# Performance work log

Measured on AMD Instinct MI355X. Metric: run time of the kernel, lower is better.

## Reference

```python
import jax, jax.numpy as jnp
import numpy as np

N = 500000          # number of nodes/points
Q = 64              # Q_mesoscale quadrature points
XI_MIN, XI_MAX = 0.0, 70.0
MLP_DIMS = [3, 64, 64, 64, 64, 1]  # num_layers=5, hidden_dim=64
STOP = 1e-3
MAX_ITER = 100


def setup_inputs() -> dict:
    key = jax.random.key(0)
    ks = jax.random.split(key, 3 + 2 * (len(MLP_DIMS) - 1))
    inp = {
        "f_distribution": jax.random.uniform(ks[0], (N, Q), jnp.float32),
        "macro_features": jax.random.uniform(ks[1], (N, 2), jnp.float32),
        "position_embedding": jax.random.normal(ks[2], (N, 1), jnp.float32),
    }
    for i in range(len(MLP_DIMS) - 1):
        din, dout = MLP_DIMS[i], MLP_DIMS[i + 1]
        scale = 1.0 / np.sqrt(din)
        inp[f"W{i}"] = jax.random.uniform(ks[3 + 2 * i], (dout, din), jnp.float32, -scale, scale)
        inp[f"b{i}"] = jax.random.uniform(ks[4 + 2 * i], (dout,), jnp.float32, -scale, scale)
    return inp


def _solve_lambda_mu(v, xi, xi2, stop=STOP, max_iter=MAX_ITER):
    # Newton-Raphson for exponential-family equilibrium: find lambda s.t. S1/S0 == v.
    # v: [N,1], xi/xi2: [Q]. Runs entirely on-device via lax.while_loop.
    def moments(lam):
        w = jnp.exp(lam * xi)                 # [N,Q]
        S0 = w.sum(axis=1, keepdims=True)     # [N,1]
        S1 = (w * xi).sum(axis=1, keepdims=True)
        S2 = (w * xi2).sum(axis=1, keepdims=True)
        return S0, S1, S2

    lam0 = jnp.zeros_like(v)
    S0, S1, S2 = moments(lam0)
    gp = (S0 * S2 - S1 ** 2) / S0 ** 2        # variance (Newton denominator)

    def cond(state):
        i, lam, S0, S1, gp = state
        return (i < max_iter) & (jnp.max(jnp.abs(gp)) > stop)

    def body(state):
        i, lam, S0, S1, gp = state
        lam1 = lam - (S1 / S0 - v) / gp
        S0, S1, S2 = moments(lam1)
        gp = (S0 * S2 - S1 ** 2) / S0 ** 2
        return (i + 1, lam1, S0, S1, gp)

    _, lam, S0, _, _ = jax.lax.while_loop(cond, body, (0, lam0, S0, S1, gp))
    mu0 = -jnp.log(S0)
    return lam, mu0


def _tau_mlp(x, Ws, bs):
    for i, (W, b) in enumerate(zip(Ws, bs)):
        x = x @ W.T + b
        if i < len(Ws) - 1:
            x = jnp.tanh(x)
    return jnp.exp(x)  # tau [N,1]


def reference(f_distribution, macro_features, position_embedding,
              W0, b0, W1, b1, W2, b2, W3, b3, W4, b4):
    xi = jnp.linspace(XI_MIN, XI_MAX, f_distribution.shape[1]).astype(f_distribution.dtype)
    rho = f_distribution.mean(axis=1, keepdims=True)                 # [N,1]
    lam, mu0 = _solve_lambda_mu(macro_features[:, :1], xi, xi * xi)  # [N,1] each
    f_eq = rho * jnp.exp(mu0) * jnp.exp(lam * xi)                    # [N,Q]
    x = jnp.concatenate([macro_features, position_embedding], axis=-1)  # [N,3]
    tau = _tau_mlp(x, [W0, W1, W2, W3, W4], [b0, b1, b2, b3, b4])    # [N,1]
    omega = -(f_distribution - f_eq) / tau                           # [N,Q]
    return omega
```

## Files before the change

### kernel.cpp

```cpp
#include <hip/hip_runtime.h>
#include <math.h>

#define Q 64
#define NPB 256

typedef __attribute__((ext_vector_type(8))) short bf16x8;
typedef __attribute__((ext_vector_type(16))) float f32x16;
typedef __attribute__((ext_vector_type(4))) unsigned int u32x4;

union BFr { u32x4 u; bf16x8 v; };

#define MFMA32(a, b, cc) __builtin_amdgcn_mfma_f32_32x32x16_bf16(a, b, cc, 0, 0, 0)

__device__ __forceinline__ float pade_tanh(float x) {
    float xc = fminf(fmaxf(x, -4.4f), 4.4f);
    float t  = xc * xc;
    float p  = fmaf(t, fmaf(t, 21.0f, 1260.0f), 10395.0f);
    float q  = fmaf(t, fmaf(t, t + 210.0f, 4725.0f), 10395.0f);
    return (xc * p) * __builtin_amdgcn_rcpf(q);
}

__device__ __forceinline__ unsigned short bf16rne(float x) {
    unsigned u = __float_as_uint(x);
    return (unsigned short)((u + 0x7fffu + ((u >> 16) & 1u)) >> 16);
}

__device__ __forceinline__ void bf16split(float x, unsigned short& h, unsigned short& l) {
    h = bf16rne(x);
    float rest = x - __uint_as_float(((unsigned)h) << 16);
    l = bf16rne(rest);
}

__device__ __forceinline__ unsigned cvt_pk_bf16(float lo, float hi) {
    unsigned r;
    asm("v_cvt_pk_bf16_f32 %0, %1, %2" : "=v"(r) : "v"(lo), "v"(hi));
    return r;
}

__device__ __forceinline__ float sum16_dpp(float x) {
    x += __int_as_float(__builtin_amdgcn_update_dpp(0, __float_as_int(x), 0xB1,  0xF, 0xF, true));
    x += __int_as_float(__builtin_amdgcn_update_dpp(0, __float_as_int(x), 0x4E,  0xF, 0xF, true));
    x += __int_as_float(__builtin_amdgcn_update_dpp(0, __float_as_int(x), 0x124, 0xF, 0xF, true));
    x += __int_as_float(__builtin_amdgcn_update_dpp(0, __float_as_int(x), 0x128, 0xF, 0xF, true));
    return x;
}

__global__ __launch_bounds__(256)
void build_wfrag(const float* __restrict__ W0, const float* __restrict__ b0,
                 const float* __restrict__ W1, const float* __restrict__ W2,
                 const float* __restrict__ W3, unsigned short* __restrict__ ws)
{
    int idx = blockIdx.x * 256 + threadIdx.x;
    if (idx < 1536) {
        int L = idx >> 9, rem = idx & 511;
        int mtp = rem >> 8, s = (rem >> 6) & 3, lane = rem & 63;
        const float* W = (L == 0) ? W1 : (L == 1) ? W2 : W3;
        int n = 32 * mtp + (lane & 31);
        int hh2 = lane >> 5;
        #pragma unroll
        for (int i = 0; i < 8; ++i) {
            int k = 16 * s + 8 * hh2 + i;
            unsigned short hh, ll;
            bf16split(W[n * 64 + k], hh, ll);
            ws[idx * 8 + i] = hh;
            ws[12288 + idx * 8 + i] = ll;
        }
    } else if (idx < 1664) {
        int j = idx - 1536;
        int mtp = j >> 6, lane = j & 63;
        int n = 32 * mtp + (lane & 31);
        int hh2 = lane >> 5;
        #pragma unroll
        for (int i = 0; i < 8; ++i) {
            int k = 8 * hh2 + i;
            float v = (k < 3) ? W0[n * 3 + k] : ((k == 3) ? b0[n] : 0.0f);
            unsigned short hh, ll;
            bf16split(v, hh, ll);
            ws[24576 + j * 8 + i] = hh;
            ws[25600 + j * 8 + i] = ll;
        }
    }
}

#define BUILD_FRAGS(fr)                                               \
    BFr fr[4][2];                                                     \
    _Pragma("unroll")                                                 \
    for (int nt = 0; nt < 2; ++nt) {                                  \
        _Pragma("unroll")                                             \
        for (int s = 0; s < 4; ++s) {                                 \
            const int mt = s >> 1, e = 4 * (s & 1);                   \
            unsigned x1 = pk[mt][nt][e + 0], y1 = pk[mt][nt][e + 2];  \
            unsigned x2 = pk[mt][nt][e + 1], y2 = pk[mt][nt][e + 3];  \
            asm("v_permlane32_swap_b32 %0, %1" : "+v"(x1), "+v"(y1)); \
            asm("v_permlane32_swap_b32 %0, %1" : "+v"(x2), "+v"(y2)); \
            fr[s][nt].u = (u32x4){x1, x2, y1, y2};                    \
        }                                                             \
    }

__global__ __launch_bounds__(NPB, 4)
void bgk_mfma(const float* __restrict__ f,
              const float* __restrict__ macro,
              const float* __restrict__ pos,
              const float* __restrict__ b1,
              const float* __restrict__ b2,
              const float* __restrict__ b3,
              const float* __restrict__ W4,
              const float* __restrict__ b4,
              const unsigned short* __restrict__ ws,
              float* __restrict__ out, int n_nodes)
{
    __shared__ float4 s_prm[NPB];

    const int tid = threadIdx.x;
    const int wv = tid >> 6, lane = tid & 63;
    const int c5 = lane & 31, h = lane >> 5;
    const int nbase = blockIdx.x * NPB;
    const float XI_H = 70.0f / 63.0f;

    const int sub = lane >> 4;
    const int qi = (lane & 15) * 4;
    const int wbase = nbase + (wv << 6);
    float4 pre[8];
    #pragma unroll
    for (int k = 0; k < 8; ++k) {
        int n = wbase + k * 4 + sub;
        int ncl = (n < n_nodes) ? n : (n_nodes - 1);
        pre[k] = *(const float4*)(f + (size_t)ncl * Q + qi);
    }

    float lam, mu0, rgeo;
    {
        int n1 = nbase + tid;
        int nc2 = (n1 < n_nodes) ? n1 : (n_nodes - 1);
        float m0 = macro[nc2 * 2];
        rgeo = fmaxf(m0 / (m0 + XI_H), 1e-30f);
        float lr = logf(rgeo);
        lam = lr / XI_H;
        float r64 = __expf(64.0f * lr);
        mu0 = -logf((1.0f - r64) / (1.0f - rgeo));
    }

    const bf16x8* wAh = (const bf16x8*)(ws);
    const bf16x8* wAl = (const bf16x8*)(ws + 12288);
    const bf16x8* l0h = (const bf16x8*)(ws + 24576);
    const bf16x8* l0l = (const bf16x8*)(ws + 25600);
    const f32x16 zero16 = {0,0,0,0,0,0,0,0,0,0,0,0,0,0,0,0};

    unsigned pk[2][2][8];

    {
        BFr bh[2], bl[2];
        #pragma unroll
        for (int nt = 0; nt < 2; ++nt) {
            int node = nbase + (wv << 6) + 32 * nt + c5;
            if (node >= n_nodes) node = n_nodes - 1;
            float m0 = macro[node * 2], m1 = macro[node * 2 + 1], pp = pos[node];
            unsigned short h0, l0_, h1, l1_, h2, l2_;
            bf16split(m0, h0, l0_); bf16split(m1, h1, l1_); bf16split(pp, h2, l2_);
            unsigned w0h = (unsigned)h0 | ((unsigned)h1 << 16);
            unsigned w1h = (unsigned)h2 | (0x3F80u << 16);
            unsigned w0l = (unsigned)l0_ | ((unsigned)l1_ << 16);
            unsigned w1l = (unsigned)l2_;
            bh[nt].u = (u32x4){ h ? 0u : w0h, h ? 0u : w1h, 0u, 0u };
            bl[nt].u = (u32x4){ h ? 0u : w0l, h ? 0u : w1l, 0u, 0u };
        }
        #pragma unroll
        for (int mtp = 0; mtp < 2; ++mtp) {
            bf16x8 Ah = l0h[mtp * 64 + lane];
            bf16x8 Al = l0l[mtp * 64 + lane];
            #pragma unroll
            for (int nt = 0; nt < 2; ++nt) {
                f32x16 t = zero16;
                t = MFMA32(Ah, bh[nt].v, t);
                t = MFMA32(Al, bh[nt].v, t);
                t = MFMA32(Ah, bl[nt].v, t);
                #pragma unroll
                for (int p = 0; p < 8; ++p)
                    pk[mtp][nt][p] = cvt_pk_bf16(pade_tanh(t[2 * p]), pade_tanh(t[2 * p + 1]));
            }
        }
    }

#define HIDDEN(Lc, BIAS)                                                       \
    {                                                                          \
        BUILD_FRAGS(fr)                                                        \
        _Pragma("unroll")                                                      \
        for (int mtp = 0; mtp < 2; ++mtp) {                                    \
            f32x16 a0;                                                         \
            _Pragma("unroll")                                                  \
            for (int j = 0; j < 4; ++j) {                                      \
                float4 bv = *(const float4*)&(BIAS)[32 * mtp + 8 * j + 4 * h]; \
                a0[4 * j + 0] = bv.x; a0[4 * j + 1] = bv.y;                    \
                a0[4 * j + 2] = bv.z; a0[4 * j + 3] = bv.w;                    \
            }                                                                  \
            f32x16 a1 = a0;                                                    \
            _Pragma("unroll")                                                  \
            for (int s = 0; s < 4; ++s) {                                      \
                const int fo = (((Lc) * 2 + mtp) * 4 + s) * 64 + lane;         \
                bf16x8 Ah = wAh[fo], Al = wAl[fo];                             \
                a0 = MFMA32(Ah, fr[s][0].v, a0);                               \
                a0 = MFMA32(Al, fr[s][0].v, a0);                               \
                a1 = MFMA32(Ah, fr[s][1].v, a1);                               \
                a1 = MFMA32(Al, fr[s][1].v, a1);                               \
            }                                                                  \
            _Pragma("unroll")                                                  \
            for (int j = 0; j < 4; ++j) {                                      \
                float v0 = pade_tanh(a0[4 * j + 0]);                           \
                float v1 = pade_tanh(a0[4 * j + 1]);                           \
                float v2 = pade_tanh(a0[4 * j + 2]);                           \
                float v3 = pade_tanh(a0[4 * j + 3]);                           \
                pk[mtp][0][2 * j + 0] = cvt_pk_bf16(v0, v1);                   \
                pk[mtp][0][2 * j + 1] = cvt_pk_bf16(v2, v3);                   \
                float u0 = pade_tanh(a1[4 * j + 0]);                           \
                float u1 = pade_tanh(a1[4 * j + 1]);                           \
                float u2 = pade_tanh(a1[4 * j + 2]);                           \
                float u3 = pade_tanh(a1[4 * j + 3]);                           \
                pk[mtp][1][2 * j + 0] = cvt_pk_bf16(u0, u1);                   \
                pk[mtp][1][2 * j + 1] = cvt_pk_bf16(u2, u3);                   \
            }                                                                  \
        }                                                                      \
    }

    HIDDEN(0, b1)
    HIDDEN(1, b2)

    {
        BUILD_FRAGS(fr)
        float zp0 = 0.f, zp1 = 0.f;
        #pragma unroll
        for (int mtp = 0; mtp < 2; ++mtp) {
            f32x16 a0;
            #pragma unroll
            for (int j = 0; j < 4; ++j) {
                float4 bv = *(const float4*)&b3[32 * mtp + 8 * j + 4 * h];
                a0[4 * j + 0] = bv.x; a0[4 * j + 1] = bv.y;
                a0[4 * j + 2] = bv.z; a0[4 * j + 3] = bv.w;
            }
            f32x16 a1 = a0;
            #pragma unroll
            for (int s = 0; s < 4; ++s) {
                const int fo = ((2 * 2 + mtp) * 4 + s) * 64 + lane;
                bf16x8 Ah = wAh[fo], Al = wAl[fo];
                a0 = MFMA32(Ah, fr[s][0].v, a0);
                a0 = MFMA32(Al, fr[s][0].v, a0);
                a1 = MFMA32(Ah, fr[s][1].v, a1);
                a1 = MFMA32(Al, fr[s][1].v, a1);
            }
            #pragma unroll
            for (int j = 0; j < 4; ++j) {
                float4 w4v = *(const float4*)&W4[32 * mtp + 8 * j + 4 * h];
                zp0 = fmaf(w4v.x, pade_tanh(a0[4 * j + 0]), zp0);
                zp0 = fmaf(w4v.y, pade_tanh(a0[4 * j + 1]), zp0);
                zp0 = fmaf(w4v.z, pade_tanh(a0[4 * j + 2]), zp0);
                zp0 = fmaf(w4v.w, pade_tanh(a0[4 * j + 3]), zp0);
                zp1 = fmaf(w4v.x, pade_tanh(a1[4 * j + 0]), zp1);
                zp1 = fmaf(w4v.y, pade_tanh(a1[4 * j + 1]), zp1);
                zp1 = fmaf(w4v.z, pade_tanh(a1[4 * j + 2]), zp1);
                zp1 = fmaf(w4v.w, pade_tanh(a1[4 * j + 3]), zp1);
            }
        }
        const float b4s = b4[0];
        zp0 += __shfl_xor(zp0, 32, 64);
        zp1 += __shfl_xor(zp1, 32, 64);
        float it0 = __expf(-(zp0 + b4s));
        float it1 = __expf(-(zp1 + b4s));
        float it  = h ? it1 : it0;
        s_prm[tid] = (float4){ it, lam, mu0, rgeo };
    }

    const float x0 = (float)qi * XI_H;
    {
        float4 fr2[8];
        #pragma unroll
        for (int k = 0; k < 8; ++k) {
            int n = wbase + (8 + k) * 4 + sub;
            int ncl = (n < n_nodes) ? n : (n_nodes - 1);
            fr2[k] = *(const float4*)(f + (size_t)ncl * Q + qi);
        }
        #pragma unroll
        for (int kb = 0; kb < 2; ++kb) {
            #pragma unroll
            for (int k = 0; k < 8; ++k) {
                const int local = (kb * 8 + k) * 4 + sub;
                const int n = wbase + local;
                const float4 fv = kb ? fr2[k] : pre[k];

                const float s = sum16_dpp(fv.x + fv.y + fv.z + fv.w);
                const float rho = s * (1.0f / 64.0f);

                const float4 prm = s_prm[(wv << 6) + local];

                const float e0 = rho * __expf(fmaf(prm.y, x0, prm.z));
                const float e1 = e0 * prm.w;
                const float e2 = e1 * prm.w;
                const float e3 = e2 * prm.w;

                float4 o;
                o.x = (e0 - fv.x) * prm.x;
                o.y = (e1 - fv.y) * prm.x;
                o.z = (e2 - fv.z) * prm.x;
                o.w = (e3 - fv.w) * prm.x;

                if (n < n_nodes) *(float4*)(out + (size_t)n * Q + qi) = o;
            }
        }
    }
}

extern "C" void kernel_launch(void* const* d_in, const int* in_sizes, int n_in,
                              void* d_out, int out_size, void* d_ws, size_t ws_size,
                              hipStream_t stream) {
    const float* f     = (const float*)d_in[0];
    const float* macro = (const float*)d_in[1];
    const float* pos   = (const float*)d_in[2];
    const float* W0 = (const float*)d_in[3];  const float* b0 = (const float*)d_in[4];
    const float* W1 = (const float*)d_in[5];  const float* b1 = (const float*)d_in[6];
    const float* W2 = (const float*)d_in[7];  const float* b2 = (const float*)d_in[8];
    const float* W3 = (const float*)d_in[9];  const float* b3 = (const float*)d_in[10];
    const float* W4 = (const float*)d_in[11]; const float* b4 = (const float*)d_in[12];
    float* out = (float*)d_out;
    unsigned short* ws = (unsigned short*)d_ws;

    const int n_nodes = in_sizes[0] / Q;
    build_wfrag<<<7, 256, 0, stream>>>(W0, b0, W1, W2, W3, ws);

    const int blocks = (n_nodes + NPB - 1) / NPB;
    bgk_mfma<<<blocks, NPB, 0, stream>>>(f, macro, pos,
                                         b1, b2, b3, W4, b4, ws,
                                         out, n_nodes);
}
```

Before: 84.06 us.

## Use single-wave blocks and pair tanh reciprocals to share one rcp

Shrinks each block from four waves to one wave of 64 nodes and drops the per-wave indexing, so blocks are smaller and can be scheduled more finely. The Pade tanh is evaluated two values at a time, with one reciprocal of the product of the denominators shared between them, which cuts the number of rcp instructions in the MLP epilogues. Combining the denominators can slightly change rounding or overflow behaviour for large inputs, although the inputs are clamped. Smaller blocks also mean four times as many blocks to launch, and the launch-bounds occupancy hint now covers far fewer threads per CU.

```diff
diff --git a/kernel.cpp b/kernel.cpp
--- a/kernel.cpp
+++ b/kernel.cpp
@@ -2,7 +2,7 @@
 #include <math.h>
 
 #define Q 64
-#define NPB 256
+#define NPB 64
 
 typedef __attribute__((ext_vector_type(8))) short bf16x8;
 typedef __attribute__((ext_vector_type(16))) float f32x16;
@@ -12,12 +12,17 @@
 
 #define MFMA32(a, b, cc) __builtin_amdgcn_mfma_f32_32x32x16_bf16(a, b, cc, 0, 0, 0)
 
-__device__ __forceinline__ float pade_tanh(float x) {
-    float xc = fminf(fmaxf(x, -4.4f), 4.4f);
-    float t  = xc * xc;
-    float p  = fmaf(t, fmaf(t, 21.0f, 1260.0f), 10395.0f);
-    float q  = fmaf(t, fmaf(t, t + 210.0f, 4725.0f), 10395.0f);
-    return (xc * p) * __builtin_amdgcn_rcpf(q);
+__device__ __forceinline__ void pade_tanh2(float x0, float x1, float& y0, float& y1) {
+    float c0 = fminf(fmaxf(x0, -4.4f), 4.4f);
+    float c1 = fminf(fmaxf(x1, -4.4f), 4.4f);
+    float t0 = c0 * c0, t1 = c1 * c1;
+    float p0 = fmaf(t0, fmaf(t0, 21.0f, 1260.0f), 10395.0f);
+    float p1 = fmaf(t1, fmaf(t1, 21.0f, 1260.0f), 10395.0f);
+    float q0 = fmaf(t0, fmaf(t0, t0 + 210.0f, 4725.0f), 10395.0f);
+    float q1 = fmaf(t1, fmaf(t1, t1 + 210.0f, 4725.0f), 10395.0f);
+    float rq = __builtin_amdgcn_rcpf(q0 * q1);
+    y0 = (c0 * p0) * (rq * q1);
+    y1 = (c1 * p1) * (rq * q0);
 }
 
 __device__ __forceinline__ unsigned short bf16rne(float x) {
@@ -111,26 +116,24 @@
 {
     __shared__ float4 s_prm[NPB];
 
-    const int tid = threadIdx.x;
-    const int wv = tid >> 6, lane = tid & 63;
+    const int lane = threadIdx.x & 63;
     const int c5 = lane & 31, h = lane >> 5;
     const int nbase = blockIdx.x * NPB;
     const float XI_H = 70.0f / 63.0f;
 
     const int sub = lane >> 4;
     const int qi = (lane & 15) * 4;
-    const int wbase = nbase + (wv << 6);
     float4 pre[8];
     #pragma unroll
     for (int k = 0; k < 8; ++k) {
-        int n = wbase + k * 4 + sub;
+        int n = nbase + k * 4 + sub;
         int ncl = (n < n_nodes) ? n : (n_nodes - 1);
         pre[k] = *(const float4*)(f + (size_t)ncl * Q + qi);
     }
 
     float lam, mu0, rgeo;
     {
-        int n1 = nbase + tid;
+        int n1 = nbase + lane;
         int nc2 = (n1 < n_nodes) ? n1 : (n_nodes - 1);
         float m0 = macro[nc2 * 2];
         rgeo = fmaxf(m0 / (m0 + XI_H), 1e-30f);
@@ -152,7 +155,7 @@
         BFr bh[2], bl[2];
         #pragma unroll
         for (int nt = 0; nt < 2; ++nt) {
-            int node = nbase + (wv << 6) + 32 * nt + c5;
+            int node = nbase + 32 * nt + c5;
             if (node >= n_nodes) node = n_nodes - 1;
             float m0 = macro[node * 2], m1 = macro[node * 2 + 1], pp = pos[node];
             unsigned short h0, l0_, h1, l1_, h2, l2_;
@@ -175,8 +178,11 @@
                 t = MFMA32(Al, bh[nt].v, t);
                 t = MFMA32(Ah, bl[nt].v, t);
                 #pragma unroll
-                for (int p = 0; p < 8; ++p)
-                    pk[mtp][nt][p] = cvt_pk_bf16(pade_tanh(t[2 * p]), pade_tanh(t[2 * p + 1]));
+                for (int p = 0; p < 8; ++p) {
+                    float y0, y1;
+                    pade_tanh2(t[2 * p], t[2 * p + 1], y0, y1);
+                    pk[mtp][nt][p] = cvt_pk_bf16(y0, y1);
+                }
             }
         }
     }
@@ -205,16 +211,14 @@
             }                                                                  \
             _Pragma("unroll")                                                  \
             for (int j = 0; j < 4; ++j) {                                      \
-                float v0 = pade_tanh(a0[4 * j + 0]);                           \
-                float v1 = pade_tanh(a0[4 * j + 1]);                           \
-                float v2 = pade_tanh(a0[4 * j + 2]);                           \
-                float v3 = pade_tanh(a0[4 * j + 3]);                           \
+                float v0, v1, v2, v3;                                          \
+                pade_tanh2(a0[4 * j + 0], a0[4 * j + 1], v0, v1);              \
+                pade_tanh2(a0[4 * j + 2], a0[4 * j + 3], v2, v3);              \
                 pk[mtp][0][2 * j + 0] = cvt_pk_bf16(v0, v1);                   \
                 pk[mtp][0][2 * j + 1] = cvt_pk_bf16(v2, v3);                   \
-                float u0 = pade_tanh(a1[4 * j + 0]);                           \
-                float u1 = pade_tanh(a1[4 * j + 1]);                           \
-                float u2 = pade_tanh(a1[4 * j + 2]);                           \
-                float u3 = pade_tanh(a1[4 * j + 3]);                           \
+                float u0, u1, u2, u3;                                          \
+                pade_tanh2(a1[4 * j + 0], a1[4 * j + 1], u0, u1);              \
+                pade_tanh2(a1[4 * j + 2], a1[4 * j + 3], u2, u3);              \
                 pk[mtp][1][2 * j + 0] = cvt_pk_bf16(u0, u1);                   \
                 pk[mtp][1][2 * j + 1] = cvt_pk_bf16(u2, u3);                   \
             }                                                                  \
@@ -249,14 +253,20 @@
             #pragma unroll
             for (int j = 0; j < 4; ++j) {
                 float4 w4v = *(const float4*)&W4[32 * mtp + 8 * j + 4 * h];
-                zp0 = fmaf(w4v.x, pade_tanh(a0[4 * j + 0]), zp0);
-                zp0 = fmaf(w4v.y, pade_tanh(a0[4 * j + 1]), zp0);
-                zp0 = fmaf(w4v.z, pade_tanh(a0[4 * j + 2]), zp0);
-                zp0 = fmaf(w4v.w, pade_tanh(a0[4 * j + 3]), zp0);
-                zp1 = fmaf(w4v.x, pade_tanh(a1[4 * j + 0]), zp1);
-                zp1 = fmaf(w4v.y, pade_tanh(a1[4 * j + 1]), zp1);
-                zp1 = fmaf(w4v.z, pade_tanh(a1[4 * j + 2]), zp1);
-                zp1 = fmaf(w4v.w, pade_tanh(a1[4 * j + 3]), zp1);
+                float s0, s1, s2, s3;
+                pade_tanh2(a0[4 * j + 0], a0[4 * j + 1], s0, s1);
+                pade_tanh2(a0[4 * j + 2], a0[4 * j + 3], s2, s3);
+                zp0 = fmaf(w4v.x, s0, zp0);
+                zp0 = fmaf(w4v.y, s1, zp0);
+                zp0 = fmaf(w4v.z, s2, zp0);
+                zp0 = fmaf(w4v.w, s3, zp0);
+                float r0, r1, r2, r3;
+                pade_tanh2(a1[4 * j + 0], a1[4 * j + 1], r0, r1);
+                pade_tanh2(a1[4 * j + 2], a1[4 * j + 3], r2, r3);
+                zp1 = fmaf(w4v.x, r0, zp1);
+                zp1 = fmaf(w4v.y, r1, zp1);
+                zp1 = fmaf(w4v.z, r2, zp1);
+                zp1 = fmaf(w4v.w, r3, zp1);
             }
         }
         const float b4s = b4[0];
@@ -265,7 +275,7 @@
         float it0 = __expf(-(zp0 + b4s));
         float it1 = __expf(-(zp1 + b4s));
         float it  = h ? it1 : it0;
-        s_prm[tid] = (float4){ it, lam, mu0, rgeo };
+        s_prm[lane] = (float4){ it, lam, mu0, rgeo };
     }
 
     const float x0 = (float)qi * XI_H;
@@ -273,7 +283,7 @@
         float4 fr2[8];
         #pragma unroll
         for (int k = 0; k < 8; ++k) {
-            int n = wbase + (8 + k) * 4 + sub;
+            int n = nbase + (8 + k) * 4 + sub;
             int ncl = (n < n_nodes) ? n : (n_nodes - 1);
             fr2[k] = *(const float4*)(f + (size_t)ncl * Q + qi);
         }
@@ -282,13 +292,13 @@
             #pragma unroll
             for (int k = 0; k < 8; ++k) {
                 const int local = (kb * 8 + k) * 4 + sub;
-                const int n = wbase + local;
+                const int n = nbase + local;
                 const float4 fv = kb ? fr2[k] : pre[k];
 
                 const float s = sum16_dpp(fv.x + fv.y + fv.z + fv.w);
                 const float rho = s * (1.0f / 64.0f);
 
-                const float4 prm = s_prm[(wv << 6) + local];
+                const float4 prm = s_prm[local];
 
                 const float e0 = rho * __expf(fmaf(prm.y, x0, prm.z));
                 const float e1 = e0 * prm.w;
```

Result: faster. 79.78 us, median of 2 (-5.1%).
